# Performance work log

Measured on AMD Instinct MI355X. Metric: run time of the kernel, lower is better.

## Reference

```python
import jax, jax.numpy as jnp
import numpy as np

N_NODES = 100000
N_EDGES = 1600000
IN_FEATS = 128
N_HIDDEN = 128
N_CLASSES = 16
INIT_EPS = 0.0
N_GIN_LAYERS = 4  # n_layers + 1


def setup_inputs() -> dict:
    key = jax.random.key(0)
    ks = jax.random.split(key, 16)
    features = jax.random.normal(ks[0], (N_NODES, IN_FEATS), dtype=jnp.float32)
    src = jax.random.randint(ks[1], (N_EDGES,), 0, N_NODES, dtype=jnp.int64)
    dst = jax.random.randint(ks[2], (N_EDGES,), 0, N_NODES, dtype=jnp.int64)
    def linear(k, fin, fout):
        bound = 1.0 / np.sqrt(fin)
        kw, kb = jax.random.split(k)
        W = jax.random.uniform(kw, (fin, fout), jnp.float32, -bound, bound)
        b = jax.random.uniform(kb, (fout,), jnp.float32, -bound, bound)
        return W, b
    W0, b0 = linear(ks[3], IN_FEATS, N_HIDDEN)
    W1, b1 = linear(ks[4], N_HIDDEN, N_HIDDEN)
    W2, b2 = linear(ks[5], N_HIDDEN, N_HIDDEN)
    W3, b3 = linear(ks[6], N_HIDDEN, N_CLASSES)
    eps = jnp.full((N_GIN_LAYERS,), INIT_EPS, dtype=jnp.float32)
    return {"features": features, "src": src, "dst": dst,
            "W0": W0, "b0": b0, "W1": W1, "b1": b1,
            "W2": W2, "b2": b2, "W3": W3, "b3": b3, "eps": eps}


def _mean_agg(h, src, dst, inv_deg):
    # gather neighbor features along edges, sum into dst, divide by in-degree
    agg = jax.ops.segment_sum(h[src], dst, num_segments=N_NODES)
    return agg * inv_deg


def _gin_layer(h, src, dst, inv_deg, eps, W, b, relu):
    z = (1.0 + eps) * h + _mean_agg(h, src, dst, inv_deg)
    out = z @ W + b  # Dropout is identity in eval mode
    return jax.nn.relu(out) if relu else out


def reference(features, src, dst, W0, b0, W1, b1, W2, b2, W3, b3, eps):
    deg = jax.ops.segment_sum(jnp.ones((src.shape[0],), features.dtype), dst,
                              num_segments=N_NODES)
    inv_deg = (1.0 / jnp.maximum(deg, 1.0))[:, None]
    h = _gin_layer(features, src, dst, inv_deg, eps[0], W0, b0, relu=True)
    h = _gin_layer(h, src, dst, inv_deg, eps[1], W1, b1, relu=True)
    h = _gin_layer(h, src, dst, inv_deg, eps[2], W2, b2, relu=True)
    h = _gin_layer(h, src, dst, inv_deg, eps[3], W3, b3, relu=False)
    return h
```

## Files before the change

kernel.cpp:

```cpp
#include <hip/hip_runtime.h>

#define NODES 100000
#define EDGES 1600000
#define FEATS 128
#define NCLS  16

#define BSH    6
#define BNODES 64
#define NB     ((NODES + BNODES - 1) / BNODES)
#define CHUNK  8192
#define NBLK   ((EDGES + CHUNK - 1) / CHUNK)
#define NHIST  (NB * NBLK)
#define BCAP   2048

typedef unsigned int  u32;
typedef unsigned short u16;
typedef __attribute__((ext_vector_type(8))) short short8;
typedef __attribute__((ext_vector_type(4))) float f32x4;

__device__ __forceinline__ float b2f(u16 v){ return __uint_as_float(((u32)v)<<16); }
__device__ __forceinline__ u16 f2b(float f){
  u32 u = __float_as_uint(f);
  u += 0x7fffu + ((u>>16)&1u);
  return (u16)(u>>16);
}
__device__ __forceinline__ float blo(u32 p){ return __uint_as_float(p<<16); }
__device__ __forceinline__ float bhi(u32 p){ return __uint_as_float(p & 0xffff0000u); }
__device__ __forceinline__ u32 pk2(float lo, float hi){
  return (u32)f2b(lo) | ((u32)f2b(hi) << 16);
}


__global__ __launch_bounds__(256) void pA_k(const int* __restrict__ dst,
                                            int* __restrict__ gh, int E){
  __shared__ int hist[NB];
  int t = threadIdx.x, blk = blockIdx.x;
  for (int j = t; j < NB; j += 256) hist[j] = 0;
  __syncthreads();
  int e0 = blk*CHUNK, e1 = e0 + CHUNK; if (e1 > E) e1 = E;
  for (int e = e0 + t; e < e1; e += 256) atomicAdd(&hist[dst[e] >> BSH], 1);
  __syncthreads();
  for (int j = t; j < NB; j += 256) gh[j*NBLK + blk] = hist[j];
}


__global__ __launch_bounds__(256) void scan1_k(const int* __restrict__ in, int* __restrict__ out,
                                               int* __restrict__ bsum, int n){
  __shared__ int sh[256];
  int t = threadIdx.x;
  int base = blockIdx.x*2048 + t*8;
  int v[8]; int s = 0;
  #pragma unroll
  for (int j=0;j<8;++j) v[j] = (base+j < n) ? in[base+j] : 0;
  #pragma unroll
  for (int j=0;j<8;++j){ int tmp = v[j]; v[j] = s; s += tmp; }
  sh[t] = s; __syncthreads();
  for (int off=1; off<256; off<<=1){
    int x = (t>=off) ? sh[t-off] : 0;
    __syncthreads();
    sh[t] += x;
    __syncthreads();
  }
  int excl = sh[t] - s;
  #pragma unroll
  for (int j=0;j<8;++j) if (base+j < n) out[base+j] = excl + v[j];
  if (t == 255) bsum[blockIdx.x] = sh[255];
}

__global__ __launch_bounds__(256) void scan2_k(const int* __restrict__ bsum,
                                               int* __restrict__ boff, int nb){
  __shared__ int sh[256];
  int t = threadIdx.x;
  int v = (t < nb) ? bsum[t] : 0;
  sh[t] = v; __syncthreads();
  for (int off=1; off<256; off<<=1){
    int x = (t>=off) ? sh[t-off] : 0;
    __syncthreads();
    sh[t] += x;
    __syncthreads();
  }
  if (t < nb) boff[t] = sh[t] - v;
}

__global__ void scan3_k(int* __restrict__ gscan, const int* __restrict__ boff,
                        int* __restrict__ bstart, int n){
  int i = blockIdx.x*256 + threadIdx.x;
  if (i < n){
    int v = gscan[i] + boff[i>>11];
    gscan[i] = v;
    if (i % NBLK == 0) bstart[i / NBLK] = v;
    if (i == 0) bstart[NB] = EDGES;
  }
}


__global__ __launch_bounds__(256) void pC_k(const int* __restrict__ src,
    const int* __restrict__ dst, const int* __restrict__ gscan,
    u32* __restrict__ elist, int E){
  __shared__ int A[NB];
  __shared__ int B[NB];
  __shared__ int sp[256];
  __shared__ u32 pay[CHUNK];
  __shared__ u16 bkt[CHUNK];
  int t = threadIdx.x, blk = blockIdx.x;
  for (int j = t; j < NB; j += 256) A[j] = 0;
  __syncthreads();
  int e0 = blk*CHUNK, e1 = e0 + CHUNK; if (e1 > E) e1 = E;
  int cnt = e1 - e0;
  for (int e = e0 + t; e < e1; e += 256) atomicAdd(&A[dst[e] >> BSH], 1);
  __syncthreads();
  {
    int base = t*7;
    int cv[7]; int s = 0;
    #pragma unroll
    for (int j=0;j<7;++j){ int idx = base+j; cv[j] = (idx < NB) ? A[idx] : 0; s += cv[j]; }
    sp[t] = s; __syncthreads();
    for (int off=1; off<256; off<<=1){
      int x = (t>=off) ? sp[t-off] : 0;
      __syncthreads();
      sp[t] += x;
      __syncthreads();
    }
    int run = sp[t] - s;
    #pragma unroll
    for (int j=0;j<7;++j){
      int idx = base+j;
      if (idx < NB){ A[idx] = run; B[idx] = run; run += cv[j]; }
    }
  }
  __syncthreads();
  for (int j = t; j < NB; j += 256) A[j] = gscan[j*NBLK + blk] - A[j];
  __syncthreads();
  for (int e = e0 + t; e < e1; e += 256){
    int d = dst[e];
    int b = d >> BSH;
    u32 w = ((u32)(d & (BNODES-1)) << 17) | (u32)src[e];
    int r = atomicAdd(&B[b], 1);
    pay[r] = w; bkt[r] = (u16)b;
  }
  __syncthreads();
  for (int i = t; i < cnt; i += 256){
    int b = bkt[i];
    elist[i + A[b]] = pay[i];
  }
}


__global__ __launch_bounds__(256) void csr_k(u32* __restrict__ elist,
    const int* __restrict__ bstart, int* __restrict__ offs, int* __restrict__ degs,
    float* __restrict__ invd, int M){
  __shared__ int hist[BNODES];
  __shared__ int pos[BNODES];
  __shared__ u32 buf[BCAP];
  __shared__ u32 buf2[BCAP];
  int b = blockIdx.x, t = threadIdx.x;
  if (t < BNODES) hist[t] = 0;
  __syncthreads();
  int s0 = bstart[b];
  int cnt = bstart[b+1] - s0; if (cnt > BCAP) cnt = BCAP;
  u32* el = elist + s0;
  for (int e = t; e < cnt; e += 256){
    u32 w = el[e];
    buf[e] = w;
    atomicAdd(&hist[w>>17], 1);
  }
  __syncthreads();
  if (t < BNODES){
    int v = hist[t];
    int s = v;
    for (int off = 1; off < BNODES; off <<= 1){
      int x = __shfl_up(s, off);
      if (t >= off) s += x;
    }
    int excl = s - v;
    pos[t] = excl;
    int node = b*BNODES + t;
    if (node < M){
      offs[node] = s0 + excl;
      degs[node] = v;
      invd[node] = 1.f / fmaxf((float)v, 1.f);
    }
  }
  __syncthreads();
  for (int e = t; e < cnt; e += 256){
    u32 w = buf[e];
    int p = atomicAdd(&pos[w>>17], 1);
    buf2[p] = w & 0x1FFFFu;
  }
  __syncthreads();
  for (int e = t; e < cnt; e += 256) el[e] = buf2[e];
}


__global__ void convf_k(const float* __restrict__ in, u16* __restrict__ o, int n4){
  int i = blockIdx.x*256 + threadIdx.x;
  if (i < n4){
    float4 x = ((const float4*)in)[i];
    ushort4 r;
    r.x = f2b(x.x); r.y = f2b(x.y); r.z = f2b(x.z); r.w = f2b(x.w);
    ((ushort4*)o)[i] = r;
  }
}

__global__ void convw_k(const float* __restrict__ W, u16* __restrict__ Wt, int Kd, int Nd){
  int i = blockIdx.x*256 + threadIdx.x;
  if (i < Kd*Nd){
    int k = i / Nd, nn = i - k*Nd;
    Wt[nn*Kd + k] = f2b(W[i]);
  }
}


template<int NT>
__global__ __launch_bounds__(256) void gemm_k(const u16* __restrict__ h,
                                              const u16* __restrict__ Wt,
                                              u16* __restrict__ y, int M){
  const int K = FEATS;
  const int N = NT*16;
  int lane = threadIdx.x & 63;
  int wave = threadIdx.x >> 6;
  int m    = lane & 15;
  int quad = lane >> 4;
  int row0 = (blockIdx.x*4 + wave)*16;
  if (row0 >= M) return;
  int rowA = row0 + m; if (rowA > M-1) rowA = M-1;
  const u16* pa = h + (size_t)rowA*K + quad*8;

  f32x4 acc[NT];
  #pragma unroll
  for (int j=0;j<NT;++j) acc[j] = (f32x4){0.f,0.f,0.f,0.f};

  #pragma unroll
  for (int kk=0; kk<K; kk+=32){
    short8 a = *(const short8*)(pa + kk);
    #pragma unroll
    for (int j=0;j<NT;++j){
      short8 b = *(const short8*)(Wt + (size_t)(j*16 + m)*K + kk + quad*8);
      acc[j] = __builtin_amdgcn_mfma_f32_16x16x32_bf16(a, b, acc[j], 0, 0, 0);
    }
  }

  #pragma unroll
  for (int j=0;j<NT;++j){
    #pragma unroll
    for (int r=0;r<4;++r){
      int row = row0 + quad*4 + r;
      if (row < M) y[(size_t)row*N + j*16 + m] = f2b(acc[j][r]);
    }
  }
}


__global__ __launch_bounds__(256) void aggL2_k(const u16* __restrict__ y,
    const u32* __restrict__ el, const int* __restrict__ offs,
    const int* __restrict__ degs, const float* __restrict__ invd,
    const float* __restrict__ bias, const float* __restrict__ epsv, int ei,
    u16* __restrict__ hout, int M){
  int lane = threadIdx.x & 63;
  int v = blockIdx.x*4 + (threadIdx.x >> 6);
  if (v >= M) return;
  int g = lane >> 4;
  int c = lane & 15;
  const uint4* y16 = (const uint4*)y;
  int start = offs[v], deg = degs[v];
  float a0=0.f,a1=0.f,a2=0.f,a3=0.f,a4=0.f,a5=0.f,a6=0.f,a7=0.f;
  for (int eb = 0; eb < deg; eb += 64){
    int nn = deg - eb; if (nn > 64) nn = 64;
    int my = (lane < nn) ? (int)el[start + eb + lane] : 0;
    int nq = nn >> 2;
    int q = 0;
    for (; q + 4 <= nq; q += 4){
      int s0 = __shfl(my, 4*q      + g);
      int s1 = __shfl(my, 4*q + 4  + g);
      int s2 = __shfl(my, 4*q + 8  + g);
      int s3 = __shfl(my, 4*q + 12 + g);
      uint4 p0 = y16[(size_t)s0*16 + c];
      uint4 p1 = y16[(size_t)s1*16 + c];
      uint4 p2 = y16[(size_t)s2*16 + c];
      uint4 p3 = y16[(size_t)s3*16 + c];
      a0 += blo(p0.x)+blo(p1.x)+blo(p2.x)+blo(p3.x);
      a1 += bhi(p0.x)+bhi(p1.x)+bhi(p2.x)+bhi(p3.x);
      a2 += blo(p0.y)+blo(p1.y)+blo(p2.y)+blo(p3.y);
      a3 += bhi(p0.y)+bhi(p1.y)+bhi(p2.y)+bhi(p3.y);
      a4 += blo(p0.z)+blo(p1.z)+blo(p2.z)+blo(p3.z);
      a5 += bhi(p0.z)+bhi(p1.z)+bhi(p2.z)+bhi(p3.z);
      a6 += blo(p0.w)+blo(p1.w)+blo(p2.w)+blo(p3.w);
      a7 += bhi(p0.w)+bhi(p1.w)+bhi(p2.w)+bhi(p3.w);
    }
    for (; q < nq; ++q){
      int s = __shfl(my, 4*q + g);
      uint4 p = y16[(size_t)s*16 + c];
      a0 += blo(p.x); a1 += bhi(p.x); a2 += blo(p.y); a3 += bhi(p.y);
      a4 += blo(p.z); a5 += bhi(p.z); a6 += blo(p.w); a7 += bhi(p.w);
    }
    int rem = nn & 3;
    if (rem){
      int idx = 4*nq + g;
      bool valid = idx < nn;
      int s = __shfl(my, valid ? idx : 0);
      uint4 p = y16[(size_t)s*16 + c];
      if (valid){
        a0 += blo(p.x); a1 += bhi(p.x); a2 += blo(p.y); a3 += bhi(p.y);
        a4 += blo(p.z); a5 += bhi(p.z); a6 += blo(p.w); a7 += bhi(p.w);
      }
    }
  }
  a0 += __shfl_xor(a0,16); a1 += __shfl_xor(a1,16); a2 += __shfl_xor(a2,16); a3 += __shfl_xor(a3,16);
  a4 += __shfl_xor(a4,16); a5 += __shfl_xor(a5,16); a6 += __shfl_xor(a6,16); a7 += __shfl_xor(a7,16);
  a0 += __shfl_xor(a0,32); a1 += __shfl_xor(a1,32); a2 += __shfl_xor(a2,32); a3 += __shfl_xor(a3,32);
  a4 += __shfl_xor(a4,32); a5 += __shfl_xor(a5,32); a6 += __shfl_xor(a6,32); a7 += __shfl_xor(a7,32);

  uint4 pv = y16[(size_t)v*16 + c];
  float4 bi0 = ((const float4*)bias)[2*c];
  float4 bi1 = ((const float4*)bias)[2*c+1];
  float inv = invd[v], e1s = 1.f + epsv[ei];
  float o0 = fmaxf(e1s*blo(pv.x) + inv*a0 + bi0.x, 0.f);
  float o1 = fmaxf(e1s*bhi(pv.x) + inv*a1 + bi0.y, 0.f);
  float o2 = fmaxf(e1s*blo(pv.y) + inv*a2 + bi0.z, 0.f);
  float o3 = fmaxf(e1s*bhi(pv.y) + inv*a3 + bi0.w, 0.f);
  float o4 = fmaxf(e1s*blo(pv.z) + inv*a4 + bi1.x, 0.f);
  float o5 = fmaxf(e1s*bhi(pv.z) + inv*a5 + bi1.y, 0.f);
  float o6 = fmaxf(e1s*blo(pv.w) + inv*a6 + bi1.z, 0.f);
  float o7 = fmaxf(e1s*bhi(pv.w) + inv*a7 + bi1.w, 0.f);
  if (g == 0){
    uint4 r;
    r.x = pk2(o0,o1); r.y = pk2(o2,o3); r.z = pk2(o4,o5); r.w = pk2(o6,o7);
    ((uint4*)hout)[(size_t)v*16 + c] = r;
  }
}


__global__ __launch_bounds__(256) void aggF2_k(const u16* __restrict__ y,
    const u32* __restrict__ el, const int* __restrict__ offs,
    const int* __restrict__ degs, const float* __restrict__ invd,
    const float* __restrict__ bias, const float* __restrict__ epsv,
    float* __restrict__ out, int M){
  int lane = threadIdx.x & 63;
  int v = blockIdx.x*4 + (threadIdx.x >> 6);
  if (v >= M) return;
  int sub = lane >> 3;
  int f2  = lane & 7;
  const u32* y2 = (const u32*)y;
  int start = offs[v], deg = degs[v];
  float acc0 = 0.f, acc1 = 0.f;
  for (int e = sub; e < deg; e += 8){
    u32 s = el[start + e];
    u32 p = y2[(size_t)s*8 + f2];
    acc0 += blo(p); acc1 += bhi(p);
  }
  acc0 += __shfl_xor(acc0, 8);  acc1 += __shfl_xor(acc1, 8);
  acc0 += __shfl_xor(acc0, 16); acc1 += __shfl_xor(acc1, 16);
  acc0 += __shfl_xor(acc0, 32); acc1 += __shfl_xor(acc1, 32);
  if (sub == 0){
    u32 pv = y2[(size_t)v*8 + f2];
    float2 bi = ((const float2*)bias)[f2];
    float e1s = 1.f + epsv[3];
    float inv = invd[v];
    out[(size_t)v*NCLS + 2*f2    ] = e1s*blo(pv) + inv*acc0 + bi.x;
    out[(size_t)v*NCLS + 2*f2 + 1] = e1s*bhi(pv) + inv*acc1 + bi.y;
  }
}


extern "C" void kernel_launch(void* const* d_in, const int* in_sizes, int n_in,
                              void* d_out, int out_size, void* d_ws, size_t ws_size,
                              hipStream_t stream){
  const float* feats = (const float*)d_in[0];
  const int*   src   = (const int*)d_in[1];
  const int*   dst   = (const int*)d_in[2];
  const float* W0 = (const float*)d_in[3];  const float* b0 = (const float*)d_in[4];
  const float* W1 = (const float*)d_in[5];  const float* b1 = (const float*)d_in[6];
  const float* W2 = (const float*)d_in[7];  const float* b2 = (const float*)d_in[8];
  const float* W3 = (const float*)d_in[9];  const float* b3 = (const float*)d_in[10];
  const float* eps = (const float*)d_in[11];

  char* w = (char*)d_ws;
  auto alloc = [&](size_t bytes)->char*{
    char* p = w; w += (bytes + 255) & ~(size_t)255; return p;
  };
  int*  gh    = (int*)alloc(sizeof(int)*NHIST);
  int*  gscan = (int*)alloc(sizeof(int)*NHIST);
  int*  bsum  = (int*)alloc(sizeof(int)*256);
  int*  boff  = (int*)alloc(sizeof(int)*256);
  int*  bstart= (int*)alloc(sizeof(int)*(NB+1));
  int*  offs  = (int*)alloc(sizeof(int)*NODES);
  int*  degs  = (int*)alloc(sizeof(int)*NODES);
  float* invd = (float*)alloc(sizeof(float)*NODES);
  u32*  elist = (u32*)alloc(sizeof(u32)*EDGES);
  u16*  hb    = (u16*)alloc(sizeof(u16)*(size_t)NODES*FEATS);
  u16*  yb    = (u16*)alloc(sizeof(u16)*(size_t)NODES*FEATS);
  u16*  Wt0   = (u16*)alloc(sizeof(u16)*128*128);
  u16*  Wt1   = (u16*)alloc(sizeof(u16)*128*128);
  u16*  Wt2   = (u16*)alloc(sizeof(u16)*128*128);
  u16*  Wt3   = (u16*)alloc(sizeof(u16)*16*128);

  pA_k<<<NBLK, 256, 0, stream>>>(dst, gh, EDGES);
  int snb = (NHIST + 2047)/2048;
  scan1_k<<<snb, 256, 0, stream>>>(gh, gscan, bsum, NHIST);
  scan2_k<<<1, 256, 0, stream>>>(bsum, boff, snb);
  scan3_k<<<(NHIST+255)/256, 256, 0, stream>>>(gscan, boff, bstart, NHIST);
  pC_k<<<NBLK, 256, 0, stream>>>(src, dst, gscan, elist, EDGES);
  csr_k<<<NB, 256, 0, stream>>>(elist, bstart, offs, degs, invd, NODES);

  convf_k<<<((NODES*FEATS/4)+255)/256, 256, 0, stream>>>(feats, hb, NODES*FEATS/4);
  convw_k<<<(128*128+255)/256, 256, 0, stream>>>(W0, Wt0, 128, 128);
  convw_k<<<(128*128+255)/256, 256, 0, stream>>>(W1, Wt1, 128, 128);
  convw_k<<<(128*128+255)/256, 256, 0, stream>>>(W2, Wt2, 128, 128);
  convw_k<<<(128*16 +255)/256, 256, 0, stream>>>(W3, Wt3, 128, 16);

  int gblocks = (NODES + 63)/64;
  int ablocks = (NODES + 3)/4;

  gemm_k<8><<<gblocks, 256, 0, stream>>>(hb, Wt0, yb, NODES);
  aggL2_k<<<ablocks, 256, 0, stream>>>(yb, elist, offs, degs, invd, b0, eps, 0, hb, NODES);
  gemm_k<8><<<gblocks, 256, 0, stream>>>(hb, Wt1, yb, NODES);
  aggL2_k<<<ablocks, 256, 0, stream>>>(yb, elist, offs, degs, invd, b1, eps, 1, hb, NODES);
  gemm_k<8><<<gblocks, 256, 0, stream>>>(hb, Wt2, yb, NODES);
  aggL2_k<<<ablocks, 256, 0, stream>>>(yb, elist, offs, degs, invd, b2, eps, 2, hb, NODES);

  gemm_k<1><<<gblocks, 256, 0, stream>>>(hb, Wt3, yb, NODES);
  aggF2_k<<<ablocks, 256, 0, stream>>>(yb, elist, offs, degs, invd, b3, eps, (float*)d_out, NODES);
}
```

Measured before the change: 508.0 us.

## Aggregate neighbor features via MFMA one-hot matrices over 16-node groups

Replaces the per-node wave gather-sum aggregation with a kernel where each wave handles 16 consecutive destination nodes. Neighbor rows are loaded straight into LDS with global_load_lds and read back with transposed LDS reads. The sum is done by an MFMA against a one-hot bf16 selection matrix built from the destination ids, which are now kept in the upper bits of the edge list. This aims to turn the scattered scalar accumulation into matrix instructions with coalesced edge streaming over the group's whole edge range. The cost is extra MFMA work on mostly-zero matrices, a full vmcnt wait on each step, and a less coalesced epilogue that loads and stores per element.

```diff
diff --git a/kernel.cpp b/kernel.cpp
--- a/kernel.cpp
+++ b/kernel.cpp
@@ -12,9 +12,11 @@
 #define NBLK   ((EDGES + CHUNK - 1) / CHUNK)
 #define NHIST  (NB * NBLK)
 #define BCAP   2048
+#define NGRP   ((NODES + 15) / 16)
 
 typedef unsigned int  u32;
 typedef unsigned short u16;
+typedef unsigned long long u64;
 typedef __attribute__((ext_vector_type(8))) short short8;
 typedef __attribute__((ext_vector_type(4))) float f32x4;
 
@@ -26,8 +28,11 @@
 }
 __device__ __forceinline__ float blo(u32 p){ return __uint_as_float(p<<16); }
 __device__ __forceinline__ float bhi(u32 p){ return __uint_as_float(p & 0xffff0000u); }
-__device__ __forceinline__ u32 pk2(float lo, float hi){
-  return (u32)f2b(lo) | ((u32)f2b(hi) << 16);
+
+__device__ __forceinline__ void gload16(const u16* g, u16* l){
+  __builtin_amdgcn_global_load_lds(
+      (const __attribute__((address_space(1))) u32*)g,
+      (__attribute__((address_space(3))) u32*)l, 16, 0, 0);
 }
 
 
@@ -154,6 +159,7 @@
   __shared__ u32 buf[BCAP];
   __shared__ u32 buf2[BCAP];
   int b = blockIdx.x, t = threadIdx.x;
+  if (b == 0 && t == 0) offs[M] = EDGES;
   if (t < BNODES) hist[t] = 0;
   __syncthreads();
   int s0 = bstart[b];
@@ -185,7 +191,7 @@
   for (int e = t; e < cnt; e += 256){
     u32 w = buf[e];
     int p = atomicAdd(&pos[w>>17], 1);
-    buf2[p] = w & 0x1FFFFu;
+    buf2[p] = w;
   }
   __syncthreads();
   for (int e = t; e < cnt; e += 256) el[e] = buf2[e];
@@ -251,81 +257,97 @@
 }
 
 
-__global__ __launch_bounds__(256) void aggL2_k(const u16* __restrict__ y,
+#define TRRD(dstv, lit) asm volatile("ds_read_b64_tr_b16 %0, %1 offset:" lit \
+                                     : "=v"(dstv) : "v"(trb2))
+
+__global__ __launch_bounds__(256) void aggM_k(const u16* __restrict__ y,
     const u32* __restrict__ el, const int* __restrict__ offs,
-    const int* __restrict__ degs, const float* __restrict__ invd,
-    const float* __restrict__ bias, const float* __restrict__ epsv, int ei,
-    u16* __restrict__ hout, int M){
+    const float* __restrict__ invd, const float* __restrict__ bias,
+    const float* __restrict__ epsv, int ei, u16* __restrict__ hout){
+  __shared__ __align__(128) u16 ybuf[4][4096];
   int lane = threadIdx.x & 63;
-  int v = blockIdx.x*4 + (threadIdx.x >> 6);
-  if (v >= M) return;
-  int g = lane >> 4;
-  int c = lane & 15;
-  const uint4* y16 = (const uint4*)y;
-  int start = offs[v], deg = degs[v];
-  float a0=0.f,a1=0.f,a2=0.f,a3=0.f,a4=0.f,a5=0.f,a6=0.f,a7=0.f;
-  for (int eb = 0; eb < deg; eb += 64){
-    int nn = deg - eb; if (nn > 64) nn = 64;
-    int my = (lane < nn) ? (int)el[start + eb + lane] : 0;
-    int nq = nn >> 2;
-    int q = 0;
-    for (; q + 4 <= nq; q += 4){
-      int s0 = __shfl(my, 4*q      + g);
-      int s1 = __shfl(my, 4*q + 4  + g);
-      int s2 = __shfl(my, 4*q + 8  + g);
-      int s3 = __shfl(my, 4*q + 12 + g);
-      uint4 p0 = y16[(size_t)s0*16 + c];
-      uint4 p1 = y16[(size_t)s1*16 + c];
-      uint4 p2 = y16[(size_t)s2*16 + c];
-      uint4 p3 = y16[(size_t)s3*16 + c];
-      a0 += blo(p0.x)+blo(p1.x)+blo(p2.x)+blo(p3.x);
-      a1 += bhi(p0.x)+bhi(p1.x)+bhi(p2.x)+bhi(p3.x);
-      a2 += blo(p0.y)+blo(p1.y)+blo(p2.y)+blo(p3.y);
-      a3 += bhi(p0.y)+bhi(p1.y)+bhi(p2.y)+bhi(p3.y);
-      a4 += blo(p0.z)+blo(p1.z)+blo(p2.z)+blo(p3.z);
-      a5 += bhi(p0.z)+bhi(p1.z)+bhi(p2.z)+bhi(p3.z);
-      a6 += blo(p0.w)+blo(p1.w)+blo(p2.w)+blo(p3.w);
-      a7 += bhi(p0.w)+bhi(p1.w)+bhi(p2.w)+bhi(p3.w);
-    }
-    for (; q < nq; ++q){
-      int s = __shfl(my, 4*q + g);
-      uint4 p = y16[(size_t)s*16 + c];
-      a0 += blo(p.x); a1 += bhi(p.x); a2 += blo(p.y); a3 += bhi(p.y);
-      a4 += blo(p.z); a5 += bhi(p.z); a6 += blo(p.w); a7 += bhi(p.w);
-    }
-    int rem = nn & 3;
-    if (rem){
-      int idx = 4*nq + g;
-      bool valid = idx < nn;
-      int s = __shfl(my, valid ? idx : 0);
-      uint4 p = y16[(size_t)s*16 + c];
-      if (valid){
-        a0 += blo(p.x); a1 += bhi(p.x); a2 += blo(p.y); a3 += bhi(p.y);
-        a4 += blo(p.z); a5 += bhi(p.z); a6 += blo(p.w); a7 += bhi(p.w);
-      }
-    }
-  }
-  a0 += __shfl_xor(a0,16); a1 += __shfl_xor(a1,16); a2 += __shfl_xor(a2,16); a3 += __shfl_xor(a3,16);
-  a4 += __shfl_xor(a4,16); a5 += __shfl_xor(a5,16); a6 += __shfl_xor(a6,16); a7 += __shfl_xor(a7,16);
-  a0 += __shfl_xor(a0,32); a1 += __shfl_xor(a1,32); a2 += __shfl_xor(a2,32); a3 += __shfl_xor(a3,32);
-  a4 += __shfl_xor(a4,32); a5 += __shfl_xor(a5,32); a6 += __shfl_xor(a6,32); a7 += __shfl_xor(a7,32);
-
-  uint4 pv = y16[(size_t)v*16 + c];
-  float4 bi0 = ((const float4*)bias)[2*c];
-  float4 bi1 = ((const float4*)bias)[2*c+1];
-  float inv = invd[v], e1s = 1.f + epsv[ei];
-  float o0 = fmaxf(e1s*blo(pv.x) + inv*a0 + bi0.x, 0.f);
-  float o1 = fmaxf(e1s*bhi(pv.x) + inv*a1 + bi0.y, 0.f);
-  float o2 = fmaxf(e1s*blo(pv.y) + inv*a2 + bi0.z, 0.f);
-  float o3 = fmaxf(e1s*bhi(pv.y) + inv*a3 + bi0.w, 0.f);
-  float o4 = fmaxf(e1s*blo(pv.z) + inv*a4 + bi1.x, 0.f);
-  float o5 = fmaxf(e1s*bhi(pv.z) + inv*a5 + bi1.y, 0.f);
-  float o6 = fmaxf(e1s*blo(pv.w) + inv*a6 + bi1.z, 0.f);
-  float o7 = fmaxf(e1s*bhi(pv.w) + inv*a7 + bi1.w, 0.f);
-  if (g == 0){
-    uint4 r;
-    r.x = pk2(o0,o1); r.y = pk2(o2,o3); r.z = pk2(o4,o5); r.w = pk2(o6,o7);
-    ((uint4*)hout)[(size_t)v*16 + c] = r;
+  int wave = threadIdx.x >> 6;
+  int grp = blockIdx.x*4 + wave;
+  if (grp >= NGRP) return;
+  int v0 = grp << 4;
+  int m    = lane & 15;
+  int quad = lane >> 4;
+  u32 tgt = (u32)(((grp & 3) << 4) + m);
+
+  u16* lb = &ybuf[wave][0];
+  typedef __attribute__((address_space(3))) u16 lds_u16;
+  u32 lbaddr = (u32)(size_t)(lds_u16*)lb;
+  u32 trb2 = lbaddr + (u32)(quad*2048) + (u32)(m*8);
+
+  int rsel = (lane & 7) >> 1;
+  int gcol = ((lane >> 3) << 4) + ((lane & 1) << 3);
+
+  int e0 = offs[v0];
+  int e1 = offs[v0 + 16];
+  int nstep = (e1 - e0 + 31) >> 5;
+
+  f32x4 acc[8];
+  #pragma unroll
+  for (int cb=0;cb<8;++cb) acc[cb] = (f32x4){0.f,0.f,0.f,0.f};
+
+  for (int st = 0; st < nstep; ++st){
+    int idx = e0 + (st<<5) + (lane & 31);
+    u32 w = (idx < e1) ? el[idx] : 0xFFFE0000u;
+
+    #pragma unroll
+    for (int i=0;i<8;++i){
+      u32 ws = (u32)__shfl((int)w, 4*i + rsel);
+      int srow = (int)(ws & 0x1FFFFu);
+      gload16(y + ((size_t)srow << 7) + gcol, lb + i*512);
+    }
+
+    union { u32 wv[4]; short8 s; } au;
+    #pragma unroll
+    for (int p=0;p<4;++p){
+      u32 w0 = (u32)__shfl((int)w, quad*8 + 2*p);
+      u32 w1 = (u32)__shfl((int)w, quad*8 + 2*p + 1);
+      au.wv[p] = (((w0>>17) == tgt) ? 0x3F80u : 0u)
+               | (((w1>>17) == tgt) ? 0x3F800000u : 0u);
+    }
+
+    asm volatile("s_waitcnt vmcnt(0)" ::: "memory");
+    __builtin_amdgcn_sched_barrier(0);
+
+    u64 t[16];
+    TRRD(t[0],  "0");    TRRD(t[1],  "1024");
+    TRRD(t[2],  "128");  TRRD(t[3],  "1152");
+    TRRD(t[4],  "256");  TRRD(t[5],  "1280");
+    TRRD(t[6],  "384");  TRRD(t[7],  "1408");
+    TRRD(t[8],  "512");  TRRD(t[9],  "1536");
+    TRRD(t[10], "640");  TRRD(t[11], "1664");
+    TRRD(t[12], "768");  TRRD(t[13], "1792");
+    TRRD(t[14], "896");  TRRD(t[15], "1920");
+    asm volatile("s_waitcnt lgkmcnt(0)" ::: "memory");
+    __builtin_amdgcn_sched_barrier(0);
+
+    #pragma unroll
+    for (int cb=0;cb<8;++cb){
+      union { u64 d[2]; short8 s; } bu;
+      bu.d[0] = t[2*cb]; bu.d[1] = t[2*cb+1];
+      acc[cb] = __builtin_amdgcn_mfma_f32_16x16x32_bf16(au.s, bu.s, acc[cb], 0, 0, 0);
+    }
+  }
+
+  float myinv = invd[v0 + m];
+  float invr[4];
+  #pragma unroll
+  for (int r=0;r<4;++r) invr[r] = __shfl(myinv, quad*4 + r);
+  float e1s = 1.f + epsv[ei];
+  #pragma unroll
+  for (int cb=0;cb<8;++cb){
+    float bi = bias[cb*16 + m];
+    #pragma unroll
+    for (int r=0;r<4;++r){
+      size_t off = (size_t)(v0 + quad*4 + r)*FEATS + cb*16 + m;
+      float self = b2f(y[off]);
+      float o = fmaxf(e1s*self + invr[r]*acc[cb][r] + bi, 0.f);
+      hout[off] = f2b(o);
+    }
   }
 }
 
@@ -344,7 +366,7 @@
   int start = offs[v], deg = degs[v];
   float acc0 = 0.f, acc1 = 0.f;
   for (int e = sub; e < deg; e += 8){
-    u32 s = el[start + e];
+    u32 s = el[start + e] & 0x1FFFFu;
     u32 p = y2[(size_t)s*8 + f2];
     acc0 += blo(p); acc1 += bhi(p);
   }
@@ -383,7 +405,7 @@
   int*  bsum  = (int*)alloc(sizeof(int)*256);
   int*  boff  = (int*)alloc(sizeof(int)*256);
   int*  bstart= (int*)alloc(sizeof(int)*(NB+1));
-  int*  offs  = (int*)alloc(sizeof(int)*NODES);
+  int*  offs  = (int*)alloc(sizeof(int)*(NODES+1));
   int*  degs  = (int*)alloc(sizeof(int)*NODES);
   float* invd = (float*)alloc(sizeof(float)*NODES);
   u32*  elist = (u32*)alloc(sizeof(u32)*EDGES);
@@ -409,14 +431,15 @@
   convw_k<<<(128*16 +255)/256, 256, 0, stream>>>(W3, Wt3, 128, 16);
 
   int gblocks = (NODES + 63)/64;
+  int mblocks = (NGRP + 3)/4;
   int ablocks = (NODES + 3)/4;
 
   gemm_k<8><<<gblocks, 256, 0, stream>>>(hb, Wt0, yb, NODES);
-  aggL2_k<<<ablocks, 256, 0, stream>>>(yb, elist, offs, degs, invd, b0, eps, 0, hb, NODES);
+  aggM_k<<<mblocks, 256, 0, stream>>>(yb, elist, offs, invd, b0, eps, 0, hb);
   gemm_k<8><<<gblocks, 256, 0, stream>>>(hb, Wt1, yb, NODES);
-  aggL2_k<<<ablocks, 256, 0, stream>>>(yb, elist, offs, degs, invd, b1, eps, 1, hb, NODES);
+  aggM_k<<<mblocks, 256, 0, stream>>>(yb, elist, offs, invd, b1, eps, 1, hb);
   gemm_k<8><<<gblocks, 256, 0, stream>>>(hb, Wt2, yb, NODES);
-  aggL2_k<<<ablocks, 256, 0, stream>>>(yb, elist, offs, degs, invd, b2, eps, 2, hb, NODES);
+  aggM_k<<<mblocks, 256, 0, stream>>>(yb, elist, offs, invd, b2, eps, 2, hb);
 
   gemm_k<1><<<gblocks, 256, 0, stream>>>(hb, Wt3, yb, NODES);
   aggF2_k<<<ablocks, 256, 0, stream>>>(yb, elist, offs, degs, invd, b3, eps, (float*)d_out, NODES);
```

New measurement: 505.3 us. Within noise of the previous version (-0.5%).
